# Optimization experiments

Measured on AMD Instinct MI355X. Metric: run time of the kernel, lower is better.

## Reference

```python
import jax, jax.numpy as jnp
import numpy as np

B, T, C, H = 2, 2048, 1024, 16
WINDOW = 512
SOFTCAP = 30.0


def setup_inputs() -> dict:
    key = jax.random.key(0)
    ks = jax.random.split(key, 4)
    s = 0.02
    return {
        "x": jax.random.normal(ks[0], (B, T, C), dtype=jnp.float32),
        "suffix_prefix_length": jax.random.randint(ks[1], (B,), 0, 256),
        "W_qkv": jax.random.normal(ks[2], (3 * C, C), dtype=jnp.float32) * s,
        "b_qkv": jnp.zeros((3 * C,), dtype=jnp.float32),
        "W_proj": jax.random.normal(ks[3], (C, C), dtype=jnp.float32) * s,
        "b_proj": jnp.zeros((C,), dtype=jnp.float32),
    }


def reference(x, suffix_prefix_length, W_qkv, b_qkv, W_proj, b_proj):
    Bb, Tt, Cc = x.shape
    d = Cc // H
    # fused qkv projection (torch Linear: x @ W.T + b)
    qkv = x @ W_qkv.T + b_qkv
    q, k, v = jnp.split(qkv, 3, axis=-1)
    q = q.reshape(Bb, Tt, H, d).transpose(0, 2, 1, 3)  # [B,H,T,d]
    k = k.reshape(Bb, Tt, H, d).transpose(0, 2, 1, 3)
    v = v.reshape(Bb, Tt, H, d).transpose(0, 2, 1, 3)

    scale = 1.0 / np.sqrt(d).astype(np.float32)
    scores = jnp.einsum("bhqd,bhkd->bhqk", q, k) * scale
    # tanh softcap applied to unmasked scores (flex_attention score_mod path)
    scores = jnp.tanh(scores / SOFTCAP) * SOFTCAP

    qi = jnp.arange(Tt)[:, None]
    kj = jnp.arange(Tt)[None, :]
    sliding_causal = (qi >= kj) & (qi - kj <= WINDOW)          # [T,T]
    prefix_global = kj[None, :, :] < suffix_prefix_length[:, None, None]  # [B,T,T]
    mask = sliding_causal[None, None, :, :] | prefix_global[:, None, :, :]

    scores = jnp.where(mask, scores, -jnp.inf)
    att = jax.nn.softmax(scores, axis=-1)
    y = jnp.einsum("bhqk,bhkd->bhqd", att, v)
    y = y.transpose(0, 2, 1, 3).reshape(Bb, Tt, Cc)
    return y @ W_proj.T + b_proj
```

## Files before the change

kernel.cpp:

```cpp
#include <hip/hip_runtime.h>
#include <hip/hip_bf16.h>

typedef __bf16 bf16x8 __attribute__((ext_vector_type(8)));
typedef float f32x4 __attribute__((ext_vector_type(4)));

#define DEVI __device__ __forceinline__

constexpr int B_ = 2, T_ = 2048, C_ = 1024, H_ = 16, D_ = 64;
constexpr int M_ = B_ * T_;
constexpr int K_ = C_;
constexpr int WINDOW_ = 512;
constexpr float SCALE_ = 0.125f;

DEVI unsigned short f2bf(float f) {
  return __builtin_bit_cast(unsigned short, (__bf16)f);
}

DEVI void gl_lds16(const unsigned short* g, unsigned short* l) {
  __builtin_amdgcn_global_load_lds(
      (const __attribute__((address_space(1))) unsigned int*)g,
      (__attribute__((address_space(3))) unsigned int*)l, 16, 0, 0);
}

__global__ void cvt_f32_bf16(const float* __restrict__ in,
                             unsigned short* __restrict__ out, int n4) {
  int i = blockIdx.x * blockDim.x + threadIdx.x;
  if (i >= n4) return;
  float4 v = reinterpret_cast<const float4*>(in)[i];
  ushort4 o;
  o.x = f2bf(v.x); o.y = f2bf(v.y); o.z = f2bf(v.z); o.w = f2bf(v.w);
  reinterpret_cast<ushort4*>(out)[i] = o;
}

template <int WHICH>
__global__ __launch_bounds__(256) void gemm_bt(
    const unsigned short* __restrict__ A, const unsigned short* __restrict__ W,
    const float* __restrict__ bias,
    unsigned short* __restrict__ oq, unsigned short* __restrict__ ok,
    unsigned short* __restrict__ ovt, float* __restrict__ of) {
  __shared__ alignas(16) unsigned short As[128 * 32];
  __shared__ alignas(16) unsigned short Bs[128 * 32];

  const int tid = threadIdx.x;
  const int n0 = blockIdx.x * 128, m0 = blockIdx.y * 128;
  const int lane = tid & 63, w = tid >> 6;
  const int wm = (w >> 1) * 64, wn = (w & 1) * 64;
  const int lr = lane & 15, lg = lane >> 4;
  const int srow = lane >> 2, scs = (lane & 3) << 3;

  f32x4 acc[4][4];
#pragma unroll
  for (int i = 0; i < 4; i++)
#pragma unroll
    for (int j = 0; j < 4; j++) acc[i][j] = f32x4{0.f, 0.f, 0.f, 0.f};

  for (int kt = 0; kt < K_; kt += 32) {
#pragma unroll
    for (int i = 0; i < 2; i++) {
      const int rb = i * 64 + w * 16;
      gl_lds16(&A[(size_t)(m0 + rb + srow) * K_ + kt + scs], &As[rb * 32]);
      gl_lds16(&W[(size_t)(n0 + rb + srow) * K_ + kt + scs], &Bs[rb * 32]);
    }
    __syncthreads();
    bf16x8 af[4], bf[4];
#pragma unroll
    for (int m = 0; m < 4; m++)
      af[m] = *reinterpret_cast<const bf16x8*>(&As[(wm + m * 16 + lr) * 32 + lg * 8]);
#pragma unroll
    for (int n = 0; n < 4; n++)
      bf[n] = *reinterpret_cast<const bf16x8*>(&Bs[(wn + n * 16 + lr) * 32 + lg * 8]);
#pragma unroll
    for (int m = 0; m < 4; m++)
#pragma unroll
      for (int n = 0; n < 4; n++)
        acc[m][n] = __builtin_amdgcn_mfma_f32_16x16x32_bf16(af[m], bf[n], acc[m][n], 0, 0, 0);
    __syncthreads();
  }

#pragma unroll
  for (int ms = 0; ms < 4; ms++) {
#pragma unroll
    for (int ns = 0; ns < 4; ns++) {
#pragma unroll
      for (int r = 0; r < 4; r++) {
        int m = m0 + wm + ms * 16 + lg * 4 + r;
        int n = n0 + wn + ns * 16 + lr;
        if constexpr (WHICH == 0) {
          float v = acc[ms][ns][r] + bias[n];
          int part = n >> 10, nc = n & 1023;
          int hh = nc >> 6, dd = nc & 63;
          int bb = m >> 11, tt = m & 2047;
          unsigned short bv = f2bf(v);
          if (part == 0)
            oq[(((size_t)(bb * H_ + hh)) * T_ + tt) * D_ + dd] = bv;
          else
            ok[(((size_t)(bb * H_ + hh)) * T_ + tt) * D_ + dd] = bv;
        } else if constexpr (WHICH == 1) {
          of[(size_t)m * C_ + n] = acc[ms][ns][r] + bias[n];
        } else {
          float v = acc[ms][ns][r] + bias[m];
          int hh = m >> 6, dd = m & 63;
          int bb = n >> 11, tt = n & 2047;
          ovt[(((size_t)(bb * H_ + hh)) * D_ + dd) * T_ + tt] = f2bf(v);
        }
      }
    }
  }
}

__global__ __launch_bounds__(256) void attn_fwd(
    const unsigned short* __restrict__ qg, const unsigned short* __restrict__ kg,
    const unsigned short* __restrict__ vtg, const int* __restrict__ spl_arr,
    unsigned short* __restrict__ out) {
  const int tid = threadIdx.x;
  const int l = tid & 63, w = tid >> 6;
  const int lr = l & 15, lg = l >> 4;

  constexpr float C1 = 0.012022458674074695f;
  constexpr float C3 = -86.56170245333781f;

  const int lin = blockIdx.x;
  const int xs = lin & 7, slot = lin >> 3;
  const int g = xs + 8 * (slot >> 5);
  const int iblk = slot & 31;
  const int b = g >> 4, h = g & 15;
  const int q_base = iblk * 64;
  const int i0 = q_base + w * 16;

  const int spl = spl_arr[b];
  const size_t bh = (size_t)(b * H_ + h);
  const unsigned short* qp = qg + bh * T_ * D_;
  const unsigned short* kp = kg + bh * T_ * D_;
  const unsigned short* vp = vtg + bh * (size_t)D_ * T_;

  __shared__ alignas(16) unsigned short Ks[64 * 64];
  __shared__ alignas(16) unsigned short Vs[64 * 64];
  __shared__ alignas(16) unsigned short Ps[4][16][80];

  bf16x8 aq0 = *reinterpret_cast<const bf16x8*>(qp + (size_t)(i0 + lr) * D_ + lg * 8);
  bf16x8 aq1 = *reinterpret_cast<const bf16x8*>(qp + (size_t)(i0 + lr) * D_ + 32 + lg * 8);

  const unsigned short one_bf = 0x3F80;
  bf16x8 ONES;
#pragma unroll
  for (int i = 0; i < 8; i++) ONES[i] = __builtin_bit_cast(__bf16, one_bf);

  f32x4 acc[4];
  f32x4 accl = f32x4{0.f, 0.f, 0.f, 0.f};
#pragma unroll
  for (int nb = 0; nb < 4; nb++) acc[nb] = f32x4{0.f, 0.f, 0.f, 0.f};

  const int pref_tiles = (spl + 63) >> 6;
  const int pref_end = pref_tiles << 6;
  int wl = q_base - WINDOW_; if (wl < 0) wl = 0; wl &= ~63;
  const int start2 = wl > pref_end ? wl : pref_end;
  const int hi = q_base + 63;
  const int n2 = (start2 <= hi) ? (((hi - start2) >> 6) + 1) : 0;
  const int ntot = pref_tiles + n2;

  const int strow = tid >> 2;
  const int c0 = (tid & 3) << 4;
  const int ssw = (strow & 7) << 3;

  for (int tb = 0; tb < ntot; tb++) {
    const int j0 = (tb < pref_tiles) ? (tb << 6) : (start2 + ((tb - pref_tiles) << 6));
    {
      const unsigned short* krow = kp + (size_t)(j0 + strow) * D_;
      const unsigned short* vrow = vp + (size_t)strow * T_ + j0;
      int4 ka0 = *reinterpret_cast<const int4*>(krow + c0);
      int4 ka1 = *reinterpret_cast<const int4*>(krow + c0 + 8);
      int4 va0 = *reinterpret_cast<const int4*>(vrow + c0);
      int4 va1 = *reinterpret_cast<const int4*>(vrow + c0 + 8);
      *reinterpret_cast<int4*>(&Ks[strow * 64 + (c0 ^ ssw)]) = ka0;
      *reinterpret_cast<int4*>(&Ks[strow * 64 + ((c0 + 8) ^ ssw)]) = ka1;
      *reinterpret_cast<int4*>(&Vs[strow * 64 + (c0 ^ ssw)]) = va0;
      *reinterpret_cast<int4*>(&Vs[strow * 64 + ((c0 + 8) ^ ssw)]) = va1;
    }
    __syncthreads();

    const bool rel = (j0 < spl) || (j0 + 63 >= i0 - WINDOW_ && j0 <= i0 + 15);
    if (rel) {
      f32x4 s[4];
#pragma unroll
      for (int ks = 0; ks < 4; ks++) {
        const int krow = ks * 16 + lr;
        const int sw = (krow & 7) << 3;
        bf16x8 b0 = *reinterpret_cast<const bf16x8*>(&Ks[krow * 64 + ((lg * 8) ^ sw)]);
        bf16x8 b1 = *reinterpret_cast<const bf16x8*>(&Ks[krow * 64 + ((32 + lg * 8) ^ sw)]);
        f32x4 t = f32x4{0.f, 0.f, 0.f, 0.f};
        t = __builtin_amdgcn_mfma_f32_16x16x32_bf16(aq0, b0, t, 0, 0, 0);
        s[ks] = __builtin_amdgcn_mfma_f32_16x16x32_bf16(aq1, b1, t, 0, 0, 0);
      }

      const bool fullv = (j0 + 63 < spl) ||
                         ((j0 + 63 <= i0) && (i0 + 15 - j0 <= WINDOW_));
      if (fullv) {
#pragma unroll
        for (int r = 0; r < 4; r++) {
          const int prow = lg * 4 + r;
#pragma unroll
          for (int ks = 0; ks < 4; ks++) {
            float t = __builtin_amdgcn_exp2f(s[ks][r] * C1);
            float p = __builtin_amdgcn_exp2f(C3 * __builtin_amdgcn_rcpf(1.0f + t));
            Ps[w][prow][ks * 16 + lr] = f2bf(p);
          }
        }
      } else {
#pragma unroll
        for (int r = 0; r < 4; r++) {
          const int prow = lg * 4 + r;
          const int irow = i0 + prow;
#pragma unroll
          for (int ks = 0; ks < 4; ks++) {
            const int jc = j0 + ks * 16 + lr;
            float t = __builtin_amdgcn_exp2f(s[ks][r] * C1);
            float p = __builtin_amdgcn_exp2f(C3 * __builtin_amdgcn_rcpf(1.0f + t));
            bool valid = (jc <= irow && irow - jc <= WINDOW_) || (jc < spl);
            p = valid ? p : 0.0f;
            Ps[w][prow][ks * 16 + lr] = f2bf(p);
          }
        }
      }

      asm volatile("s_waitcnt lgkmcnt(0)" ::: "memory");

      bf16x8 pa0 = *reinterpret_cast<const bf16x8*>(&Ps[w][lr][lg * 8]);
      bf16x8 pa1 = *reinterpret_cast<const bf16x8*>(&Ps[w][lr][32 + lg * 8]);

      accl = __builtin_amdgcn_mfma_f32_16x16x32_bf16(pa0, ONES, accl, 0, 0, 0);
      accl = __builtin_amdgcn_mfma_f32_16x16x32_bf16(pa1, ONES, accl, 0, 0, 0);

#pragma unroll
      for (int nb = 0; nb < 4; nb++) {
        const int vrow = nb * 16 + lr;
        const int sw = (vrow & 7) << 3;
        bf16x8 bv0 = *reinterpret_cast<const bf16x8*>(&Vs[vrow * 64 + ((lg * 8) ^ sw)]);
        bf16x8 bv1 = *reinterpret_cast<const bf16x8*>(&Vs[vrow * 64 + ((32 + lg * 8) ^ sw)]);
        acc[nb] = __builtin_amdgcn_mfma_f32_16x16x32_bf16(pa0, bv0, acc[nb], 0, 0, 0);
        acc[nb] = __builtin_amdgcn_mfma_f32_16x16x32_bf16(pa1, bv1, acc[nb], 0, 0, 0);
      }
    }
    __syncthreads();
  }

  float rl[4];
#pragma unroll
  for (int r = 0; r < 4; r++) rl[r] = __builtin_amdgcn_rcpf(accl[r]);
#pragma unroll
  for (int nb = 0; nb < 4; nb++) {
#pragma unroll
    for (int r = 0; r < 4; r++) {
      float o = acc[nb][r] * rl[r];
      int t = i0 + lg * 4 + r;
      out[((size_t)(b * T_ + t)) * C_ + h * D_ + nb * 16 + lr] = f2bf(o);
    }
  }
}

extern "C" void kernel_launch(void* const* d_in, const int* in_sizes, int n_in,
                              void* d_out, int out_size, void* d_ws, size_t ws_size,
                              hipStream_t stream) {
  const float* x = (const float*)d_in[0];
  const int* spl = (const int*)d_in[1];
  const float* Wqkv = (const float*)d_in[2];
  const float* bqkv = (const float*)d_in[3];
  const float* Wproj = (const float*)d_in[4];
  const float* bproj = (const float*)d_in[5];
  float* out = (float*)d_out;

  char* ws = (char*)d_ws;
  unsigned short* xb = (unsigned short*)ws;       ws += (size_t)M_ * K_ * 2;
  unsigned short* wqkvb = (unsigned short*)ws;    ws += (size_t)3 * C_ * K_ * 2;
  unsigned short* wprojb = (unsigned short*)ws;   ws += (size_t)C_ * K_ * 2;
  unsigned short* qb = (unsigned short*)ws;       ws += (size_t)M_ * C_ * 2;
  unsigned short* kb = (unsigned short*)ws;       ws += (size_t)M_ * C_ * 2;
  unsigned short* vtb = (unsigned short*)ws;      ws += (size_t)M_ * C_ * 2;
  unsigned short* ab = (unsigned short*)ws;       ws += (size_t)M_ * C_ * 2;

  {
    int n4 = (M_ * K_) / 4;
    cvt_f32_bf16<<<(n4 + 255) / 256, 256, 0, stream>>>(x, xb, n4);
  }
  {
    int n4 = (3 * C_ * K_) / 4;
    cvt_f32_bf16<<<(n4 + 255) / 256, 256, 0, stream>>>(Wqkv, wqkvb, n4);
  }
  {
    int n4 = (C_ * K_) / 4;
    cvt_f32_bf16<<<(n4 + 255) / 256, 256, 0, stream>>>(Wproj, wprojb, n4);
  }

  gemm_bt<0><<<dim3(2048 / 128, M_ / 128), 256, 0, stream>>>(
      xb, wqkvb, bqkv, qb, kb, nullptr, nullptr);

  gemm_bt<2><<<dim3(M_ / 128, 1024 / 128), 256, 0, stream>>>(
      wqkvb + (size_t)2048 * K_, xb, bqkv + 2048, nullptr, nullptr, vtb, nullptr);

  attn_fwd<<<dim3(1024), 256, 0, stream>>>(qb, kb, vtb, spl, ab);

  gemm_bt<1><<<dim3(C_ / 128, M_ / 128), 256, 0, stream>>>(
      ab, wprojb, bproj, nullptr, nullptr, nullptr, out);
}
```

Before: 191.0 us.

## Double-buffer GEMM LDS, prefetch attention K/V, swizzle blocks, merge conversion launches

The GEMM now uses two LDS buffers so the next K-slice loads while the current one feeds the MFMAs, and its workgroup indices are remapped across groups of 8 to improve L2 locality. The attention kernel prefetches the next K/V tile into registers while the current tile is being processed. The three fp32-to-bf16 conversion launches are combined into one kernel. These changes target load latency and launch overhead, at the cost of double the GEMM LDS and extra registers, which may lower occupancy.

```diff
diff --git a/kernel.cpp b/kernel.cpp
--- a/kernel.cpp
+++ b/kernel.cpp
@@ -10,7 +10,6 @@
 constexpr int M_ = B_ * T_;
 constexpr int K_ = C_;
 constexpr int WINDOW_ = 512;
-constexpr float SCALE_ = 0.125f;
 
 DEVI unsigned short f2bf(float f) {
   return __builtin_bit_cast(unsigned short, (__bf16)f);
@@ -22,14 +21,24 @@
       (__attribute__((address_space(3))) unsigned int*)l, 16, 0, 0);
 }
 
-__global__ void cvt_f32_bf16(const float* __restrict__ in,
-                             unsigned short* __restrict__ out, int n4) {
+__global__ void cvt_all(const float* __restrict__ x, const float* __restrict__ wqkv,
+                        const float* __restrict__ wproj,
+                        unsigned short* __restrict__ xb,
+                        unsigned short* __restrict__ wqkvb,
+                        unsigned short* __restrict__ wprojb) {
+  constexpr int N1 = M_ * K_ / 4, N2 = 3 * C_ * K_ / 4, N3 = C_ * K_ / 4;
   int i = blockIdx.x * blockDim.x + threadIdx.x;
-  if (i >= n4) return;
-  float4 v = reinterpret_cast<const float4*>(in)[i];
+  const float* in;
+  unsigned short* out;
+  int idx;
+  if (i < N1) { in = x; out = xb; idx = i; }
+  else if (i < N1 + N2) { in = wqkv; out = wqkvb; idx = i - N1; }
+  else if (i < N1 + N2 + N3) { in = wproj; out = wprojb; idx = i - N1 - N2; }
+  else return;
+  float4 v = reinterpret_cast<const float4*>(in)[idx];
   ushort4 o;
   o.x = f2bf(v.x); o.y = f2bf(v.y); o.z = f2bf(v.z); o.w = f2bf(v.w);
-  reinterpret_cast<ushort4*>(out)[i] = o;
+  reinterpret_cast<ushort4*>(out)[idx] = o;
 }
 
 template <int WHICH>
@@ -38,11 +47,17 @@
     const float* __restrict__ bias,
     unsigned short* __restrict__ oq, unsigned short* __restrict__ ok,
     unsigned short* __restrict__ ovt, float* __restrict__ of) {
-  __shared__ alignas(16) unsigned short As[128 * 32];
-  __shared__ alignas(16) unsigned short Bs[128 * 32];
+  __shared__ alignas(16) unsigned short As[2][128 * 32];
+  __shared__ alignas(16) unsigned short Bs[2][128 * 32];
 
   const int tid = threadIdx.x;
-  const int n0 = blockIdx.x * 128, m0 = blockIdx.y * 128;
+  const int nby = gridDim.y;
+  const int nwg = gridDim.x * nby;
+  const int orig = blockIdx.x * nby + blockIdx.y;
+  const int cpx = nwg >> 3;
+  const int swz = (orig & 7) * cpx + (orig >> 3);
+  const int n0 = (swz / nby) * 128, m0 = (swz % nby) * 128;
+
   const int lane = tid & 63, w = tid >> 6;
   const int wm = (w >> 1) * 64, wn = (w & 1) * 64;
   const int lr = lane & 15, lg = lane >> 4;
@@ -54,28 +69,41 @@
 #pragma unroll
     for (int j = 0; j < 4; j++) acc[i][j] = f32x4{0.f, 0.f, 0.f, 0.f};
 
-  for (int kt = 0; kt < K_; kt += 32) {
+  auto STAGE = [&](int buf, int kt) {
 #pragma unroll
     for (int i = 0; i < 2; i++) {
       const int rb = i * 64 + w * 16;
-      gl_lds16(&A[(size_t)(m0 + rb + srow) * K_ + kt + scs], &As[rb * 32]);
-      gl_lds16(&W[(size_t)(n0 + rb + srow) * K_ + kt + scs], &Bs[rb * 32]);
-    }
+      gl_lds16(&A[(size_t)(m0 + rb + srow) * K_ + kt + scs], &As[buf][rb * 32]);
+      gl_lds16(&W[(size_t)(n0 + rb + srow) * K_ + kt + scs], &Bs[buf][rb * 32]);
+    }
+  };
+  auto COMPUTE = [&](int buf) {
+    bf16x8 af[4], bfr[4];
+#pragma unroll
+    for (int m = 0; m < 4; m++)
+      af[m] = *reinterpret_cast<const bf16x8*>(&As[buf][(wm + m * 16 + lr) * 32 + lg * 8]);
+#pragma unroll
+    for (int n = 0; n < 4; n++)
+      bfr[n] = *reinterpret_cast<const bf16x8*>(&Bs[buf][(wn + n * 16 + lr) * 32 + lg * 8]);
+#pragma unroll
+    for (int m = 0; m < 4; m++)
+#pragma unroll
+      for (int n = 0; n < 4; n++)
+        acc[m][n] = __builtin_amdgcn_mfma_f32_16x16x32_bf16(af[m], bfr[n], acc[m][n], 0, 0, 0);
+  };
+
+  STAGE(0, 0);
+  asm volatile("s_waitcnt vmcnt(0)" ::: "memory");
+  __syncthreads();
+  int cur = 0;
+  for (int kt = 32; kt < K_; kt += 32) {
+    STAGE(cur ^ 1, kt);
+    COMPUTE(cur);
+    asm volatile("s_waitcnt vmcnt(0)" ::: "memory");
     __syncthreads();
-    bf16x8 af[4], bf[4];
-#pragma unroll
-    for (int m = 0; m < 4; m++)
-      af[m] = *reinterpret_cast<const bf16x8*>(&As[(wm + m * 16 + lr) * 32 + lg * 8]);
-#pragma unroll
-    for (int n = 0; n < 4; n++)
-      bf[n] = *reinterpret_cast<const bf16x8*>(&Bs[(wn + n * 16 + lr) * 32 + lg * 8]);
-#pragma unroll
-    for (int m = 0; m < 4; m++)
-#pragma unroll
-      for (int n = 0; n < 4; n++)
-        acc[m][n] = __builtin_amdgcn_mfma_f32_16x16x32_bf16(af[m], bf[n], acc[m][n], 0, 0, 0);
-    __syncthreads();
-  }
+    cur ^= 1;
+  }
+  COMPUTE(cur);
 
 #pragma unroll
   for (int ms = 0; ms < 4; ms++) {
@@ -162,21 +190,38 @@
   const int c0 = (tid & 3) << 4;
   const int ssw = (strow & 7) << 3;
 
+  auto J0 = [&](int tb) {
+    return (tb < pref_tiles) ? (tb << 6) : (start2 + ((tb - pref_tiles) << 6));
+  };
+
+  int4 ka0, ka1, va0, va1;
+  {
+    const int j0 = J0(0);
+    const unsigned short* krow = kp + (size_t)(j0 + strow) * D_;
+    const unsigned short* vrow = vp + (size_t)strow * T_ + j0;
+    ka0 = *reinterpret_cast<const int4*>(krow + c0);
+    ka1 = *reinterpret_cast<const int4*>(krow + c0 + 8);
+    va0 = *reinterpret_cast<const int4*>(vrow + c0);
+    va1 = *reinterpret_cast<const int4*>(vrow + c0 + 8);
+  }
+
   for (int tb = 0; tb < ntot; tb++) {
-    const int j0 = (tb < pref_tiles) ? (tb << 6) : (start2 + ((tb - pref_tiles) << 6));
-    {
-      const unsigned short* krow = kp + (size_t)(j0 + strow) * D_;
-      const unsigned short* vrow = vp + (size_t)strow * T_ + j0;
-      int4 ka0 = *reinterpret_cast<const int4*>(krow + c0);
-      int4 ka1 = *reinterpret_cast<const int4*>(krow + c0 + 8);
-      int4 va0 = *reinterpret_cast<const int4*>(vrow + c0);
-      int4 va1 = *reinterpret_cast<const int4*>(vrow + c0 + 8);
-      *reinterpret_cast<int4*>(&Ks[strow * 64 + (c0 ^ ssw)]) = ka0;
-      *reinterpret_cast<int4*>(&Ks[strow * 64 + ((c0 + 8) ^ ssw)]) = ka1;
-      *reinterpret_cast<int4*>(&Vs[strow * 64 + (c0 ^ ssw)]) = va0;
-      *reinterpret_cast<int4*>(&Vs[strow * 64 + ((c0 + 8) ^ ssw)]) = va1;
-    }
+    const int j0 = J0(tb);
+    *reinterpret_cast<int4*>(&Ks[strow * 64 + (c0 ^ ssw)]) = ka0;
+    *reinterpret_cast<int4*>(&Ks[strow * 64 + ((c0 + 8) ^ ssw)]) = ka1;
+    *reinterpret_cast<int4*>(&Vs[strow * 64 + (c0 ^ ssw)]) = va0;
+    *reinterpret_cast<int4*>(&Vs[strow * 64 + ((c0 + 8) ^ ssw)]) = va1;
     __syncthreads();
+
+    if (tb + 1 < ntot) {
+      const int j1 = J0(tb + 1);
+      const unsigned short* krow = kp + (size_t)(j1 + strow) * D_;
+      const unsigned short* vrow = vp + (size_t)strow * T_ + j1;
+      ka0 = *reinterpret_cast<const int4*>(krow + c0);
+      ka1 = *reinterpret_cast<const int4*>(krow + c0 + 8);
+      va0 = *reinterpret_cast<const int4*>(vrow + c0);
+      va1 = *reinterpret_cast<const int4*>(vrow + c0 + 8);
+    }
 
     const bool rel = (j0 < spl) || (j0 + 63 >= i0 - WINDOW_ && j0 <= i0 + 15);
     if (rel) {
@@ -278,16 +323,8 @@
   unsigned short* ab = (unsigned short*)ws;       ws += (size_t)M_ * C_ * 2;
 
   {
-    int n4 = (M_ * K_) / 4;
-    cvt_f32_bf16<<<(n4 + 255) / 256, 256, 0, stream>>>(x, xb, n4);
-  }
-  {
-    int n4 = (3 * C_ * K_) / 4;
-    cvt_f32_bf16<<<(n4 + 255) / 256, 256, 0, stream>>>(Wqkv, wqkvb, n4);
-  }
-  {
-    int n4 = (C_ * K_) / 4;
-    cvt_f32_bf16<<<(n4 + 255) / 256, 256, 0, stream>>>(Wproj, wprojb, n4);
+    constexpr int NT = (M_ * K_ + 3 * C_ * K_ + C_ * K_) / 4;
+    cvt_all<<<(NT + 255) / 256, 256, 0, stream>>>(x, Wqkv, Wproj, xb, wqkvb, wprojb);
   }
 
   gemm_bt<0><<<dim3(2048 / 128, M_ / 128), 256, 0, stream>>>(
```

New measurement: 200.0 us. 4.7% more time.
